# Performance work log

Measured on AMD Instinct MI355X. Metric: run time of the kernel, lower is better.

The kernel has to match this reference:

```python
import jax, jax.numpy as jnp
import numpy as np

PAD_IDX = 0        # assumed padding index (not defined in source snippet)
LAMBDA = 1.0       # lambda_bias buffer value
B, S, D, H = 2, 2048, 1024, 16
HD = D // H        # head_dim = 64
SCALE = HD ** -0.5


def setup_inputs() -> dict:
    key = jax.random.key(0)
    ks = jax.random.split(key, 18)
    w = lambda k: jax.random.normal(k, (D, D), jnp.float32) * 0.02
    b = lambda k: jax.random.normal(k, (D,), jnp.float32) * 0.02
    return {
        "query": jax.random.normal(ks[0], (B, S, D), jnp.float32),
        "key":   jax.random.normal(ks[1], (B, S, D), jnp.float32),
        "value": jax.random.normal(ks[2], (B, S, D), jnp.float32),
        # minval=1 for field_ids so no token is PAD -> no all--inf softmax rows
        "field_ids":      jax.random.randint(ks[3], (B, S), 1, 32),
        "entity_ids":     jax.random.randint(ks[4], (B, S), 0, 64),
        "time_ids":       jax.random.randint(ks[5], (B, S), 0, 128),
        "token_type_ids": jax.random.randint(ks[6], (B, S), 0, 8),
        "edge_ids":       jax.random.randint(ks[7], (B, S), 0, 4),
        "role_ids":       jax.random.randint(ks[8], (B, S), 0, 8),
        "Wq": w(ks[9]),  "bq": b(ks[10]),
        "Wk": w(ks[11]), "bk": b(ks[12]),
        "Wv": w(ks[13]), "bv": b(ks[14]),
        "Wo": w(ks[15]), "bo": b(ks[16]),
    }


def _bias_matrix(field_ids, entity_ids, time_ids, token_type_ids, edge_ids, role_ids):
    # pairwise equality bias, shape [B, S, S]
    eq = lambda x: (x[:, :, None] == x[:, None, :]).astype(jnp.float32)
    has_edge = ((edge_ids[:, :, None] != PAD_IDX) | (edge_ids[:, None, :] != PAD_IDX)).astype(jnp.float32)
    bias = (eq(field_ids)
            + eq(entity_ids)
            + 0.5 * eq(time_ids)
            + 0.3 * eq(token_type_ids)
            + 1.5 * has_edge
            + 0.5 * eq(role_ids))
    is_pad = field_ids == PAD_IDX
    pad_mask = is_pad[:, :, None] | is_pad[:, None, :]
    return jnp.where(pad_mask, -jnp.inf, bias)


def reference(query, key, value, field_ids, entity_ids, time_ids, token_type_ids,
              edge_ids, role_ids, Wq, bq, Wk, bk, Wv, bv, Wo, bo):
    Bsz, Sq, _ = query.shape
    Q = (query @ Wq.T + bq).reshape(Bsz, Sq, H, HD)
    K = (key   @ Wk.T + bk).reshape(Bsz, Sq, H, HD)
    V = (value @ Wv.T + bv).reshape(Bsz, Sq, H, HD)
    # [B, H, S, S]
    scores = jnp.einsum('bihd,bjhd->bhij', Q, K) * SCALE
    B_struct = _bias_matrix(field_ids, entity_ids, time_ids, token_type_ids, edge_ids, role_ids)
    scores = scores + LAMBDA * B_struct[:, None, :, :]
    attn = jax.nn.softmax(scores, axis=-1)
    out = jnp.einsum('bhij,bjhd->bihd', attn, V).reshape(Bsz, Sq, D)
    return out @ Wo.T + bo
```

## Files before the change

### kernel.cpp

```cpp
#include <hip/hip_runtime.h>
#include <hip/hip_bf16.h>
#include <stdint.h>

#define B_N 2
#define S_N 2048
#define D_N 1024
#define H_N 16
#define LOG2E 1.44269504f

using bf8    = __attribute__((ext_vector_type(8))) short;
using us8    = __attribute__((ext_vector_type(8))) unsigned short;
using f32x4  = __attribute__((ext_vector_type(4))) float;
using f32x16 = __attribute__((ext_vector_type(16))) float;

static __device__ __forceinline__ ushort f2b(float f) {
  uint32_t u = __builtin_bit_cast(uint32_t, f);
  u += 0x7fffu + ((u >> 16) & 1u);
  return (ushort)(u >> 16);
}

static __device__ __forceinline__ uint32_t cvtpk(float a, float b) {
  uint32_t r;
  asm("v_cvt_pk_bf16_f32 %0, %1, %2" : "=v"(r) : "v"(a), "v"(b));
  return r;
}

static __device__ __forceinline__ float h2f(ushort u) {
  return (float)__builtin_bit_cast(_Float16, u);
}

static __device__ __forceinline__ ushort h16(float x) {
  return __builtin_bit_cast(ushort, (_Float16)x);
}

typedef __attribute__((address_space(1))) const uint32_t GU32;
typedef __attribute__((address_space(3))) uint32_t LU32;
static __device__ __forceinline__ void gload16(const void* g, void* l) {
  __builtin_amdgcn_global_load_lds((GU32*)g, (LU32*)l, 16, 0, 0);
}

static __device__ __forceinline__ void cvt4B(const float* __restrict__ s, ushort* __restrict__ d, int i) {
  float4 v = *(const float4*)(s + i);
  ushort4 o;
  o.x = f2b(v.x); o.y = f2b(v.y); o.z = f2b(v.z); o.w = f2b(v.w);
  *(ushort4*)(d + i) = o;
}

__global__ __launch_bounds__(256) void prep_kernel(
    const float* __restrict__ q, const float* __restrict__ k, const float* __restrict__ v,
    const float* __restrict__ wq, const float* __restrict__ wk, const float* __restrict__ wv,
    const float* __restrict__ wo,
    ushort* __restrict__ oq, ushort* __restrict__ ok, ushort* __restrict__ ov,
    ushort* __restrict__ owq, ushort* __restrict__ owk, ushort* __restrict__ owv,
    ushort* __restrict__ owo,
    const int* __restrict__ f, const int* __restrict__ e, const int* __restrict__ ti,
    const int* __restrict__ tt, const int* __restrict__ ed, const int* __restrict__ ro,
    uint32_t* __restrict__ codes) {
  int x = blockIdx.x;
  if (x < 12288) {
    int which = x >> 12, i = (x & 4095) * 1024 + threadIdx.x * 4;
    const float* s = (which == 0) ? q : (which == 1) ? k : v;
    ushort* d = (which == 0) ? oq : (which == 1) ? ok : ov;
    cvt4B(s, d, i);
  } else if (x < 16384) {
    int which = (x - 12288) >> 10, i = (x & 1023) * 1024 + threadIdx.x * 4;
    const float* s = (which == 0) ? wq : (which == 1) ? wk : (which == 2) ? wv : wo;
    ushort* d = (which == 0) ? owq : (which == 1) ? owk : (which == 2) ? owv : owo;
    cvt4B(s, d, i);
  } else {
    int i = (x - 16384) * 256 + threadIdx.x;
    uint32_t c = ((uint32_t)f[i] & 31u) | (((uint32_t)e[i] & 63u) << 5) |
                 (((uint32_t)ti[i] & 127u) << 11) | (((uint32_t)tt[i] & 7u) << 18) |
                 (((uint32_t)ro[i] & 7u) << 21) |
                 ((ed[i] != 0) ? (1u << 24) : 0u) | ((f[i] == 0) ? (1u << 25) : 0u);
    codes[i] = c;
  }
}

static __device__ __forceinline__ float bias_val(uint32_t a, uint32_t b) {
  uint32_t x = a ^ b;
  uint32_t o = a | b;
  float v = (o & 0x1000000u) ? 1.5f : 0.0f;
  v += (x & 0x1Fu)     ? 0.0f : 1.0f;
  v += (x & 0x7E0u)    ? 0.0f : 1.0f;
  v += (x & 0x3F800u)  ? 0.0f : 0.5f;
  v += (x & 0x1C0000u) ? 0.0f : 0.3f;
  v += (x & 0xE00000u) ? 0.0f : 0.5f;
  return (o & 0x2000000u) ? -30000.f : v;
}

__global__ __launch_bounds__(256) void bias_build(const uint32_t* __restrict__ codes,
                                                  ushort* __restrict__ BF) {
  int t = blockIdx.x * 256 + threadIdx.x;
  int v8    = t & 1;
  int lane  = (t >> 1) & 63;
  int h     = (t >> 7) & 1;
  int kvt   = (t >> 8) & 31;
  int qtile = (t >> 13) & 63;
  int b     = t >> 19;
  int hi = lane >> 5;
  int q  = qtile * 32 + (lane & 31);
  uint32_t cq = codes[b * S_N + q];
  int kvb = kvt * 64 + h * 32 + v8 * 16 + hi * 4;
  uint4 c0 = *(const uint4*)(codes + b * S_N + kvb);
  uint4 c1 = *(const uint4*)(codes + b * S_N + kvb + 8);
  ushort o[8];
  o[0] = h16(bias_val(cq, c0.x) * LOG2E);
  o[1] = h16(bias_val(cq, c0.y) * LOG2E);
  o[2] = h16(bias_val(cq, c0.z) * LOG2E);
  o[3] = h16(bias_val(cq, c0.w) * LOG2E);
  o[4] = h16(bias_val(cq, c1.x) * LOG2E);
  o[5] = h16(bias_val(cq, c1.y) * LOG2E);
  o[6] = h16(bias_val(cq, c1.z) * LOG2E);
  o[7] = h16(bias_val(cq, c1.w) * LOG2E);
  *(uint4*)(BF + (size_t)t * 8) = *(const uint4*)o;
}

template <int MODE>
static __device__ __forceinline__ void gemm_core(ushort* As, ushort* Bs,
    const ushort* __restrict__ A, const ushort* __restrict__ W, const float* __restrict__ bias,
    void* __restrict__ out, float scale) {
  const int tid = threadIdx.x, lane = tid & 63, wid = tid >> 6;
  const int g = lane >> 4, c = lane & 15;
  const int wm = wid >> 1, wn = wid & 1;
  const int m0 = blockIdx.y * 128, n0 = blockIdx.x * 128;

  f32x4 acc[4][4];
#pragma unroll
  for (int i = 0; i < 4; ++i)
#pragma unroll
    for (int j = 0; j < 4; ++j) acc[i][j] = (f32x4){0.f, 0.f, 0.f, 0.f};

  for (int k0 = 0; k0 < D_N; k0 += 32) {
#pragma unroll
    for (int j = 0; j < 2; ++j) {
      int idx = tid + j * 256;
      int row = idx >> 2, c8 = (idx & 3) * 8;
      gload16(A + (size_t)(m0 + row) * D_N + k0 + c8, As + idx * 8);
      gload16(W + (size_t)(n0 + row) * D_N + k0 + c8, Bs + idx * 8);
    }
    __syncthreads();
    bf8 af[4], bw[4];
#pragma unroll
    for (int mi = 0; mi < 4; ++mi) af[mi] = *(const bf8*)(As + (wm * 64 + mi * 16 + c) * 32 + g * 8);
#pragma unroll
    for (int ni = 0; ni < 4; ++ni) bw[ni] = *(const bf8*)(Bs + (wn * 64 + ni * 16 + c) * 32 + g * 8);
#pragma unroll
    for (int mi = 0; mi < 4; ++mi)
#pragma unroll
      for (int ni = 0; ni < 4; ++ni)
        acc[mi][ni] = __builtin_amdgcn_mfma_f32_16x16x32_bf16(af[mi], bw[ni], acc[mi][ni], 0, 0, 0);
    __syncthreads();
  }

#pragma unroll
  for (int mi = 0; mi < 4; ++mi)
#pragma unroll
    for (int ni = 0; ni < 4; ++ni) {
      int ncol = n0 + wn * 64 + ni * 16 + c;
      float bv = bias[ncol];
      int hh = ncol >> 6, dd = ncol & 63;
      if (MODE == 2) {
        int mb = m0 + wm * 64 + mi * 16 + g * 4;
        int bb = mb >> 11, kv = mb & 2047;
        int kvt = kv >> 6, kin = kv & 63;
        int ks = kin >> 4, hif = (kin >> 3) & 1, e = kin & 7;
        int jj = dd >> 5, l31v = dd & 31;
        int lanef = hif * 32 + l31v;
        size_t off = (((size_t)(bb * H_N + hh) * 32 + kvt) * 8 + ks * 2 + jj) * 512 + lanef * 8 + e;
        ushort4 o4;
        o4.x = f2b((acc[mi][ni][0] + bv) * scale);
        o4.y = f2b((acc[mi][ni][1] + bv) * scale);
        o4.z = f2b((acc[mi][ni][2] + bv) * scale);
        o4.w = f2b((acc[mi][ni][3] + bv) * scale);
        *(ushort4*)((ushort*)out + off) = o4;
      } else {
#pragma unroll
        for (int r = 0; r < 4; ++r) {
          int m = m0 + wm * 64 + mi * 16 + g * 4 + r;
          float v = (acc[mi][ni][r] + bv) * scale;
          if (MODE == 0) {
            int bb = m >> 11, q = m & 2047;
            int qtile = q >> 5, l31q = q & 31;
            int ks = dd >> 4, hif = (dd >> 3) & 1, e = dd & 7;
            int lanef = hif * 32 + l31q;
            size_t off = (((size_t)(bb * H_N + hh) * 64 + qtile) * 4 + ks) * 512 + lanef * 8 + e;
            ((ushort*)out)[off] = f2b(v);
          } else if (MODE == 3) {
            int bb = m >> 11, s = m & 2047;
            int kvt = s >> 6, sin = s & 63;
            int jj = sin >> 5, l31k = sin & 31;
            int ks = dd >> 4, hif = (dd >> 3) & 1, e = dd & 7;
            int lanef = hif * 32 + l31k;
            size_t off = (((size_t)(bb * H_N + hh) * 32 + kvt) * 8 + ks * 2 + jj) * 512 + lanef * 8 + e;
            ((ushort*)out)[off] = f2b(v);
          } else {
            ((float*)out)[(size_t)m * D_N + ncol] = v;
          }
        }
      }
    }
}

__global__ __launch_bounds__(256) void gemm_qkv(
    const ushort* __restrict__ Xq, const ushort* __restrict__ Xk, const ushort* __restrict__ Xv,
    const ushort* __restrict__ Wq, const ushort* __restrict__ Wk, const ushort* __restrict__ Wv,
    const float* __restrict__ bq, const float* __restrict__ bk, const float* __restrict__ bv,
    ushort* __restrict__ Qo, ushort* __restrict__ Ko, ushort* __restrict__ Vo) {
  __shared__ __align__(16) ushort As[128 * 32];
  __shared__ __align__(16) ushort Bs[128 * 32];
  if (blockIdx.z == 0)      gemm_core<0>(As, Bs, Xq, Wq, bq, Qo, 0.125f * LOG2E);
  else if (blockIdx.z == 1) gemm_core<3>(As, Bs, Xk, Wk, bk, Ko, 1.0f);
  else                      gemm_core<2>(As, Bs, Xv, Wv, bv, Vo, 1.0f);
}

__global__ __launch_bounds__(256) void gemm_o(const ushort* __restrict__ A, const ushort* __restrict__ W,
                                              const float* __restrict__ bias, float* __restrict__ out) {
  __shared__ __align__(16) ushort As[128 * 32];
  __shared__ __align__(16) ushort Bs[128 * 32];
  gemm_core<1>(As, Bs, A, W, bias, out, 1.0f);
}

__global__ __launch_bounds__(256, 2) void attn_kernel(const ushort* __restrict__ QF, const ushort* __restrict__ KF,
                                                      const ushort* __restrict__ VF, const ushort* __restrict__ BF,
                                                      ushort* __restrict__ AO) {
  const int tid = threadIdx.x, lane = tid & 63, w = tid >> 6;
  const int l31 = lane & 31, hi = lane >> 5;
  const int raw = blockIdx.x;
  const int bh = (raw & 7) * 4 + ((raw >> 3) & 3);
  const int x  = raw >> 5;
  const int b = bh >> 4, h = bh & 15;
  const int qtile = x * 4 + w;

  const ushort* Qp = QF + ((size_t)(bh * 64 + qtile) * 4) * 512 + lane * 8;
  bf8 aq[4];
#pragma unroll
  for (int ks = 0; ks < 4; ++ks) aq[ks] = *(const bf8*)(Qp + ks * 512);

  const ushort* Ku = KF + (size_t)bh * 32 * 8 * 512;
  const ushort* Vu = VF + (size_t)bh * 32 * 8 * 512;
  const ushort* Bu = BF + (size_t)(b * 64 + qtile) * 32 * 2048;
  const int koff = lane * 8;
  const int boff = lane * 16;

  float lr = 0.f;
  f32x16 o0, o1;
#pragma unroll
  for (int r = 0; r < 16; ++r) { o0[r] = 0.f; o1[r] = 0.f; }

  const int CROW0[16] = {0,1,2,3, 8,9,10,11, 16,17,18,19, 24,25,26,27};

  auto LOADK = [&](bf8 (&kf)[4][2], int t) {
    const ushort* p = Ku + (size_t)t * 4096 + koff;
#pragma unroll
    for (int ks = 0; ks < 4; ++ks) {
      kf[ks][0] = *(const bf8*)(p + (ks * 2 + 0) * 512);
      kf[ks][1] = *(const bf8*)(p + (ks * 2 + 1) * 512);
    }
  };
  auto LOADV = [&](bf8 (&vf)[4][2], int t) {
    const ushort* p = Vu + (size_t)t * 4096 + koff;
#pragma unroll
    for (int ks = 0; ks < 4; ++ks) {
      vf[ks][0] = *(const bf8*)(p + (ks * 2 + 0) * 512);
      vf[ks][1] = *(const bf8*)(p + (ks * 2 + 1) * 512);
    }
  };
  auto LOADB = [&](us8 (&bb)[4], int t) {
    const ushort* p = Bu + (size_t)t * 2048 + boff;
    bb[0] = *(const us8*)(p);
    bb[1] = *(const us8*)(p + 8);
    bb[2] = *(const us8*)(p + 1024);
    bb[3] = *(const us8*)(p + 1024 + 8);
  };

  auto TILE = [&](const bf8 (&kf)[4][2], const bf8 (&vf)[4][2], const us8 (&bb)[4]) {
    f32x16 s0, s1;
#pragma unroll
    for (int g = 0; g < 4; ++g)
#pragma unroll
      for (int j = 0; j < 4; ++j) {
        s0[g * 4 + j] = h2f(bb[g >> 1][(g & 1) * 4 + j]);
        s1[g * 4 + j] = h2f(bb[2 + (g >> 1)][(g & 1) * 4 + j]);
      }
    __builtin_amdgcn_s_setprio(1);
#pragma unroll
    for (int ks = 0; ks < 4; ++ks) {
      s0 = __builtin_amdgcn_mfma_f32_32x32x16_bf16(kf[ks][0], aq[ks], s0, 0, 0, 0);
      s1 = __builtin_amdgcn_mfma_f32_32x32x16_bf16(kf[ks][1], aq[ks], s1, 0, 0, 0);
    }
    __builtin_amdgcn_s_setprio(0);

#pragma unroll
    for (int r = 0; r < 16; ++r) {
      s0[r] = __builtin_exp2f(s0[r]);
      s1[r] = __builtin_exp2f(s1[r]);
    }
    float a8[8];
#pragma unroll
    for (int r = 0; r < 8; ++r)
      a8[r] = (s0[r] + s0[r + 8]) + (s1[r] + s1[r + 8]);
    lr += ((a8[0] + a8[4]) + (a8[1] + a8[5])) + ((a8[2] + a8[6]) + (a8[3] + a8[7]));

    bf8 pa[4];
#pragma unroll
    for (int t = 0; t < 2; ++t) {
      uint32_t wv[4][2];
#pragma unroll
      for (int g = 0; g < 4; ++g) {
        const float* sp = (t == 0) ? (const float*)&s0 : (const float*)&s1;
        wv[g][0] = cvtpk(sp[g * 4 + 0], sp[g * 4 + 1]);
        wv[g][1] = cvtpk(sp[g * 4 + 2], sp[g * 4 + 3]);
      }
#pragma unroll
      for (int pr = 0; pr < 2; ++pr) {
        uint32_t x0 = hi ? wv[2 * pr][0] : wv[2 * pr + 1][0];
        uint32_t x1 = hi ? wv[2 * pr][1] : wv[2 * pr + 1][1];
        uint32_t r0 = (uint32_t)__shfl_xor((int)x0, 32);
        uint32_t r1 = (uint32_t)__shfl_xor((int)x1, 32);
        uint4 pw;
        pw.x = hi ? r0 : wv[2 * pr][0];
        pw.y = hi ? r1 : wv[2 * pr][1];
        pw.z = hi ? wv[2 * pr + 1][0] : r0;
        pw.w = hi ? wv[2 * pr + 1][1] : r1;
        pa[t * 2 + pr] = __builtin_bit_cast(bf8, pw);
      }
    }

    __builtin_amdgcn_s_setprio(1);
#pragma unroll
    for (int ks = 0; ks < 4; ++ks) {
      o0 = __builtin_amdgcn_mfma_f32_32x32x16_bf16(pa[ks], vf[ks][0], o0, 0, 0, 0);
      o1 = __builtin_amdgcn_mfma_f32_32x32x16_bf16(pa[ks], vf[ks][1], o1, 0, 0, 0);
    }
    __builtin_amdgcn_s_setprio(0);
  };

  bf8 kA[4][2], kB[4][2], vC[4][2];
  us8 bA[4], bB[4];
  LOADK(kA, 0); LOADB(bA, 0);

#pragma unroll 1
  for (int p = 0; p < 15; ++p) {
    int t = 2 * p;
    LOADK(kB, t + 1); LOADB(bB, t + 1); LOADV(vC, t);
    TILE(kA, vC, bA);
    LOADK(kA, t + 2); LOADB(bA, t + 2); LOADV(vC, t + 1);
    TILE(kB, vC, bB);
  }
  LOADK(kB, 31); LOADB(bB, 31); LOADV(vC, 30);
  TILE(kA, vC, bA);
  LOADV(vC, 31);
  TILE(kB, vC, bB);

  lr += __shfl_xor(lr, 32);
  float inv = 1.0f / lr;
#pragma unroll
  for (int r = 0; r < 16; ++r) {
    float ivr = __shfl(inv, CROW0[r] + 4 * hi);
    int q = qtile * 32 + CROW0[r] + 4 * hi;
    size_t base = ((size_t)b * S_N + q) * D_N + h * 64 + l31;
    AO[base]      = f2b(o0[r] * ivr);
    AO[base + 32] = f2b(o1[r] * ivr);
  }
}

extern "C" void kernel_launch(void* const* d_in, const int* in_sizes, int n_in,
                              void* d_out, int out_size, void* d_ws, size_t ws_size,
                              hipStream_t stream) {
  (void)in_sizes; (void)n_in; (void)out_size; (void)ws_size;
  const float* query = (const float*)d_in[0];
  const float* key_  = (const float*)d_in[1];
  const float* value = (const float*)d_in[2];
  const int* fid  = (const int*)d_in[3];
  const int* eid  = (const int*)d_in[4];
  const int* tmid = (const int*)d_in[5];
  const int* ttid = (const int*)d_in[6];
  const int* edid = (const int*)d_in[7];
  const int* rlid = (const int*)d_in[8];
  const float* Wq = (const float*)d_in[9];  const float* bq = (const float*)d_in[10];
  const float* Wk = (const float*)d_in[11]; const float* bk = (const float*)d_in[12];
  const float* Wv = (const float*)d_in[13]; const float* bv = (const float*)d_in[14];
  const float* Wo = (const float*)d_in[15]; const float* bo = (const float*)d_in[16];

  char* ws = (char*)d_ws;
  const size_t MB = 1024 * 1024;
  ushort* Xq  = (ushort*)(ws);
  ushort* Xk  = (ushort*)(ws + 8 * MB);
  ushort* Xv  = (ushort*)(ws + 16 * MB);
  ushort* Wqb = (ushort*)(ws + 24 * MB);
  ushort* Wkb = (ushort*)(ws + 26 * MB);
  ushort* Wvb = (ushort*)(ws + 28 * MB);
  ushort* BF  = (ushort*)(ws);
  ushort* QFw = (ushort*)(ws + 30 * MB);
  ushort* KFw = (ushort*)(ws + 38 * MB);
  ushort* VFw = (ushort*)(ws + 46 * MB);
  ushort* AOw = (ushort*)(ws + 54 * MB);
  ushort* Wob = (ushort*)(ws + 62 * MB);
  uint32_t* codes = (uint32_t*)(ws + 64 * MB);

  prep_kernel<<<16400, 256, 0, stream>>>(query, key_, value, Wq, Wk, Wv, Wo,
                                         Xq, Xk, Xv, Wqb, Wkb, Wvb, Wob,
                                         fid, eid, tmid, ttid, edid, rlid, codes);
  gemm_qkv<<<dim3(D_N / 128, (B_N * S_N) / 128, 3), 256, 0, stream>>>(
      Xq, Xk, Xv, Wqb, Wkb, Wvb, bq, bk, bv, QFw, KFw, VFw);
  bias_build<<<4096, 256, 0, stream>>>(codes, BF);
  attn_kernel<<<512, 256, 0, stream>>>(QFw, KFw, VFw, BF, AOw);
  gemm_o<<<dim3(D_N / 128, (B_N * S_N) / 128), 256, 0, stream>>>(AOw, Wob, bo, (float*)d_out);
}
```

Before: 156.5 us.

## Split attention key range across two waves and merge partials via LDS

Each attention block now holds two waves that share one query tile and each process half of the key/value tiles. The partial outputs and row sums are combined through shared memory before normalization. The grid grows fourfold to raise occupancy and latency hiding, at the cost of a block barrier, LDS reduction traffic and duplicated Q loads.

```diff
diff --git a/kernel.cpp b/kernel.cpp
--- a/kernel.cpp
+++ b/kernel.cpp
@@ -221,25 +221,26 @@
   gemm_core<1>(As, Bs, A, W, bias, out, 1.0f);
 }
 
-__global__ __launch_bounds__(256, 2) void attn_kernel(const ushort* __restrict__ QF, const ushort* __restrict__ KF,
+__global__ __launch_bounds__(128, 4) void attn_kernel(const ushort* __restrict__ QF, const ushort* __restrict__ KF,
                                                       const ushort* __restrict__ VF, const ushort* __restrict__ BF,
                                                       ushort* __restrict__ AO) {
+  __shared__ float Lx[2][32 * 32];
+  __shared__ float Ll[2][32];
   const int tid = threadIdx.x, lane = tid & 63, w = tid >> 6;
   const int l31 = lane & 31, hi = lane >> 5;
   const int raw = blockIdx.x;
   const int bh = (raw & 7) * 4 + ((raw >> 3) & 3);
-  const int x  = raw >> 5;
+  const int qtile = raw >> 5;
   const int b = bh >> 4, h = bh & 15;
-  const int qtile = x * 4 + w;
 
   const ushort* Qp = QF + ((size_t)(bh * 64 + qtile) * 4) * 512 + lane * 8;
   bf8 aq[4];
 #pragma unroll
   for (int ks = 0; ks < 4; ++ks) aq[ks] = *(const bf8*)(Qp + ks * 512);
 
-  const ushort* Ku = KF + (size_t)bh * 32 * 8 * 512;
-  const ushort* Vu = VF + (size_t)bh * 32 * 8 * 512;
-  const ushort* Bu = BF + (size_t)(b * 64 + qtile) * 32 * 2048;
+  const ushort* Ku = KF + (size_t)bh * 32 * 8 * 512 + (size_t)(w * 16) * 4096;
+  const ushort* Vu = VF + (size_t)bh * 32 * 8 * 512 + (size_t)(w * 16) * 4096;
+  const ushort* Bu = BF + ((size_t)(b * 64 + qtile) * 32 + w * 16) * 2048;
   const int koff = lane * 8;
   const int boff = lane * 16;
 
@@ -341,27 +342,52 @@
   LOADK(kA, 0); LOADB(bA, 0);
 
 #pragma unroll 1
-  for (int p = 0; p < 15; ++p) {
+  for (int p = 0; p < 7; ++p) {
     int t = 2 * p;
     LOADK(kB, t + 1); LOADB(bB, t + 1); LOADV(vC, t);
     TILE(kA, vC, bA);
     LOADK(kA, t + 2); LOADB(bA, t + 2); LOADV(vC, t + 1);
     TILE(kB, vC, bB);
   }
-  LOADK(kB, 31); LOADB(bB, 31); LOADV(vC, 30);
+  LOADK(kB, 15); LOADB(bB, 15); LOADV(vC, 14);
   TILE(kA, vC, bA);
-  LOADV(vC, 31);
+  LOADV(vC, 15);
   TILE(kB, vC, bB);
 
   lr += __shfl_xor(lr, 32);
-  float inv = 1.0f / lr;
-#pragma unroll
-  for (int r = 0; r < 16; ++r) {
-    float ivr = __shfl(inv, CROW0[r] + 4 * hi);
-    int q = qtile * 32 + CROW0[r] + 4 * hi;
-    size_t base = ((size_t)b * S_N + q) * D_N + h * 64 + l31;
-    AO[base]      = f2b(o0[r] * ivr);
-    AO[base + 32] = f2b(o1[r] * ivr);
+
+  if (w == 0) {
+#pragma unroll
+    for (int r = 0; r < 16; ++r)
+      Lx[0][(CROW0[r] + 4 * hi) * 32 + l31] = o1[r];
+    if (lane < 32) Ll[0][l31] = lr;
+  } else {
+#pragma unroll
+    for (int r = 0; r < 16; ++r)
+      Lx[1][(CROW0[r] + 4 * hi) * 32 + l31] = o0[r];
+    if (lane < 32) Ll[1][l31] = lr;
+  }
+  __syncthreads();
+
+  float lt = lr + Ll[1 - w][l31];
+  float inv = 1.0f / lt;
+  size_t obase = ((size_t)b * S_N + qtile * 32) * D_N + h * 64 + w * 32 + l31;
+  if (w == 0) {
+#pragma unroll
+    for (int r = 0; r < 16; ++r) {
+      int qr = CROW0[r] + 4 * hi;
+      float ivr = __shfl(inv, qr);
+      float v = o0[r] + Lx[1][qr * 32 + l31];
+      AO[obase + (size_t)qr * D_N] = f2b(v * ivr);
+    }
+  } else {
+#pragma unroll
+    for (int r = 0; r < 16; ++r) {
+      int qr = CROW0[r] + 4 * hi;
+      float ivr = __shfl(inv, qr);
+      float v = o1[r] + Lx[0][qr * 32 + l31];
+      AO[obase + (size_t)qr * D_N] = f2b(v * ivr);
+    }
   }
 }
 
@@ -405,6 +431,6 @@
   gemm_qkv<<<dim3(D_N / 128, (B_N * S_N) / 128, 3), 256, 0, stream>>>(
       Xq, Xk, Xv, Wqb, Wkb, Wvb, bq, bk, bv, QFw, KFw, VFw);
   bias_build<<<4096, 256, 0, stream>>>(codes, BF);
-  attn_kernel<<<512, 256, 0, stream>>>(QFw, KFw, VFw, BF, AOw);
+  attn_kernel<<<2048, 128, 0, stream>>>(QFw, KFw, VFw, BF, AOw);
   gemm_o<<<dim3(D_N / 128, (B_N * S_N) / 128), 256, 0, stream>>>(AOw, Wob, bo, (float*)d_out);
 }
```

Measured after the change: 364.3 us. +132.8%, slower.
